# Kernel tuning notes

Hardware: AMD Instinct MI355X
Metric: run time of the kernel (lower is better)

Reference implementation:

```python
import jax, jax.numpy as jnp
import numpy as np

NUM_EXPERTS = 8
TOP_K = 2
D_IN = 1024
D_OUT = 1024
N_TOKENS = 8192


def setup_inputs() -> dict:
    key = jax.random.key(0)
    ks = jax.random.split(key, 7)
    s_in = 1.0 / np.sqrt(D_IN)
    s_out = 1.0 / np.sqrt(D_OUT)
    return {
        "x": jax.random.normal(ks[0], (N_TOKENS, D_IN), dtype=jnp.float32),
        # stacked expert params: fc1 [E, D_in, D_out], fc2 [E, D_out, D_out]
        "W1": jax.random.uniform(ks[1], (NUM_EXPERTS, D_IN, D_OUT), jnp.float32, -s_in, s_in),
        "b1": jax.random.uniform(ks[2], (NUM_EXPERTS, D_OUT), jnp.float32, -s_in, s_in),
        "W2": jax.random.uniform(ks[3], (NUM_EXPERTS, D_OUT, D_OUT), jnp.float32, -s_out, s_out),
        "b2": jax.random.uniform(ks[4], (NUM_EXPERTS, D_OUT), jnp.float32, -s_out, s_out),
        "Wg": jax.random.uniform(ks[5], (D_IN, NUM_EXPERTS), jnp.float32, -s_in, s_in),
        "bg": jax.random.uniform(ks[6], (NUM_EXPERTS,), jnp.float32, -s_in, s_in),
    }


def reference(x, W1, b1, W2, b2, Wg, bg):
    n = x.shape[0]
    # gating
    gate_logits = x @ Wg + bg                      # [N, E]
    gate_weights = jax.nn.softmax(gate_logits, axis=1)
    if TOP_K < NUM_EXPERTS:
        topk_vals, topk_idx = jax.lax.top_k(gate_weights, TOP_K)  # [N, K]
        rows = jnp.arange(n)[:, None]
        gate_weights = jnp.zeros_like(gate_weights).at[rows, topk_idx].set(topk_vals)
    # dense all-expert MLP fan-out (faithful to the original wasteful compute)
    h = jax.nn.relu(jnp.einsum('nd,edh->enh', x, W1) + b1[:, None, :])  # [E, N, H]
    y = jnp.einsum('enh,eho->eno', h, W2) + b2[:, None, :]               # [E, N, O]
    # weighted combine over experts
    out = jnp.einsum('ne,eno->no', gate_weights, y)                      # [N, O]
    return out
```

## Files before the change

kernel.cpp:

```cpp
#include <hip/hip_runtime.h>

#define NUM_E 8
#define N_TOK 8192
#define DIM 1024

typedef __attribute__((ext_vector_type(8))) short short8;
typedef __attribute__((ext_vector_type(4))) float f32x4;

__device__ __forceinline__ unsigned short f2bf(float f) {
  unsigned int u = __float_as_uint(f);
  u = (u + 0x7fffu + ((u >> 16) & 1u)) >> 16;
  return (unsigned short)u;
}

__device__ __forceinline__ void async16(const unsigned short* g, unsigned short* l) {
  __builtin_amdgcn_global_load_lds((const __attribute__((address_space(1))) void*)g,
                                   (__attribute__((address_space(3))) void*)l,
                                   16, 0, 0);
}

__global__ __launch_bounds__(256) void prep_kernel(
    const float* __restrict__ W1, const float* __restrict__ W2,
    unsigned short* __restrict__ W1T, unsigned short* __restrict__ W2T,
    const float* __restrict__ x, const float* __restrict__ Wg,
    const float* __restrict__ bg, int* __restrict__ tok_top,
    float2* __restrict__ tok_wts, unsigned short* __restrict__ xb) {
  __shared__ float s[64][65];
  if (blockIdx.x < 4096) {
    const int bx  = blockIdx.x;
    const int mat = bx >> 8;
    const int tk  = (bx >> 4) & 15;
    const int tn  = bx & 15;
    const float* src;
    unsigned short* dst;
    if (mat < 8) { src = W1 + (size_t)mat * (DIM * DIM); dst = W1T + (size_t)mat * (DIM * DIM); }
    else         { src = W2 + (size_t)(mat - 8) * (DIM * DIM); dst = W2T + (size_t)(mat - 8) * (DIM * DIM); }
    const int k0 = tk * 64, n0 = tn * 64;
    const int t = threadIdx.x;
    const int nr = t & 63, wr = t >> 6;
#pragma unroll
    for (int i = 0; i < 16; ++i) {
      int k = i * 4 + wr;
      s[nr][k] = src[(size_t)(k0 + k) * DIM + n0 + nr];
    }
    __syncthreads();
    const int kq = (t & 15) * 4, nw = t >> 4;
#pragma unroll
    for (int i = 0; i < 4; ++i) {
      int n = i * 16 + nw;
      ushort4 o;
      o.x = f2bf(s[n][kq + 0]); o.y = f2bf(s[n][kq + 1]);
      o.z = f2bf(s[n][kq + 2]); o.w = f2bf(s[n][kq + 3]);
      *(ushort4*)(dst + (size_t)(n0 + n) * DIM + k0 + kq) = o;
    }
  } else {
    const int wave = threadIdx.x >> 6;
    const int lane = threadIdx.x & 63;
    const int n = (blockIdx.x - 4096) * 4 + wave;
    const float4* xr = (const float4*)(x + (size_t)n * DIM);
    unsigned short* xbr = xb + (size_t)n * DIM;
    float acc[NUM_E];
#pragma unroll
    for (int e = 0; e < NUM_E; ++e) acc[e] = 0.f;
#pragma unroll
    for (int it = 0; it < 4; ++it) {
      float4 xv = xr[it * 64 + lane];
      const float4* wr = (const float4*)Wg + (size_t)(it * 256 + lane * 4) * 2;
      float xs[4] = {xv.x, xv.y, xv.z, xv.w};
      union { unsigned short u[4]; uint2 v; } oo;
      oo.u[0] = f2bf(xv.x); oo.u[1] = f2bf(xv.y);
      oo.u[2] = f2bf(xv.z); oo.u[3] = f2bf(xv.w);
      *(uint2*)(xbr + it * 256 + lane * 4) = oo.v;
#pragma unroll
      for (int dd = 0; dd < 4; ++dd) {
        float4 wa = wr[dd * 2 + 0];
        float4 wb = wr[dd * 2 + 1];
        acc[0] += xs[dd] * wa.x; acc[1] += xs[dd] * wa.y;
        acc[2] += xs[dd] * wa.z; acc[3] += xs[dd] * wa.w;
        acc[4] += xs[dd] * wb.x; acc[5] += xs[dd] * wb.y;
        acc[6] += xs[dd] * wb.z; acc[7] += xs[dd] * wb.w;
      }
    }
#pragma unroll
    for (int e = 0; e < NUM_E; ++e)
#pragma unroll
      for (int off = 32; off > 0; off >>= 1)
        acc[e] += __shfl_down(acc[e], off);
    if (lane == 0) {
      float p[NUM_E];
      float mx = -1e30f;
#pragma unroll
      for (int e = 0; e < NUM_E; ++e) { p[e] = acc[e] + bg[e]; mx = fmaxf(mx, p[e]); }
      float ss = 0.f;
#pragma unroll
      for (int e = 0; e < NUM_E; ++e) { p[e] = expf(p[e] - mx); ss += p[e]; }
      float inv = 1.f / ss;
      int i0 = 0;
#pragma unroll
      for (int e = 1; e < NUM_E; ++e) if (p[e] > p[i0]) i0 = e;
      int i1 = (i0 == 0) ? 1 : 0;
#pragma unroll
      for (int e = 0; e < NUM_E; ++e) if (e != i0 && p[e] > p[i1]) i1 = e;
      tok_top[n] = i0 | (i1 << 8);
      tok_wts[n] = make_float2(p[i0] * inv, p[i1] * inv);
    }
  }
}

__global__ __launch_bounds__(1024) void gate2_kernel(const int* __restrict__ tok_top,
                                                     const float2* __restrict__ tok_wts,
                                                     int* __restrict__ counts,
                                                     int* __restrict__ tok_idx,
                                                     float* __restrict__ tok_w) {
  const int e = blockIdx.x;
  const int t = threadIdx.x;
  const int lane = t & 63;
  const int wave = t >> 6;
  __shared__ int wsum[16];
  __shared__ int blocktot;
  int match[8];
  float w[8];
  int cnt = 0;
#pragma unroll
  for (int j = 0; j < 8; ++j) {
    int n = t * 8 + j;
    int top = tok_top[n];
    float2 ww = tok_wts[n];
    bool m0 = (top & 0xff) == e;
    bool m1 = ((top >> 8) & 0xff) == e;
    match[j] = (m0 || m1) ? 1 : 0;
    w[j] = m0 ? ww.x : ww.y;
    cnt += match[j];
  }
  int inc = cnt;
#pragma unroll
  for (int off = 1; off < 64; off <<= 1) {
    int v = __shfl_up(inc, off);
    if (lane >= off) inc += v;
  }
  if (lane == 63) wsum[wave] = inc;
  __syncthreads();
  if (t < 16) {
    int v = wsum[t];
    int s = v;
#pragma unroll
    for (int off = 1; off < 16; off <<= 1) {
      int u = __shfl_up(s, off);
      if (lane >= off) s += u;
    }
    wsum[t] = s - v;
    if (t == 15) blocktot = s;
  }
  __syncthreads();
  int slot = wsum[wave] + inc - cnt;
#pragma unroll
  for (int j = 0; j < 8; ++j) {
    if (match[j]) {
      tok_idx[e * N_TOK + slot] = t * 8 + j;
      tok_w[e * N_TOK + slot] = w[j];
      slot++;
    }
  }
  if (t == 0) counts[e] = blocktot;
}


template <bool FC1>
__global__ __launch_bounds__(256, 3) void moe_gemm_kernel(
    const unsigned short* __restrict__ A_src,
    const unsigned short* __restrict__ wT,
    const float* __restrict__ bias,
    const int* __restrict__ counts,
    const int* __restrict__ tok_idx,
    const float* __restrict__ tok_w,
    unsigned short* __restrict__ h_out,
    float* __restrict__ out)
{
  const int y = blockIdx.y;
  int e = -1, m0 = 0, base = 0;
  {
    int acc_tiles = 0, acc_rows = 0;
#pragma unroll
    for (int i = 0; i < NUM_E; ++i) {
      int c = counts[i];
      int t = (c + 127) >> 7;
      if (y >= acc_tiles && y < acc_tiles + t) {
        e = i; m0 = (y - acc_tiles) * 128; base = acc_rows;
      }
      acc_tiles += t;
      acc_rows += t * 128;
    }
  }
  if (e < 0) return;
  const int count = counts[e];
  const int n0 = blockIdx.x * 128;

  const int tid  = threadIdx.x;
  const int wave = tid >> 6;
  const int lane = tid & 63;
  const int l15  = lane & 15;
  const int quad = lane >> 4;
  const int wm   = wave & 1;
  const int wn   = wave >> 1;

  __shared__ unsigned short sA[2 * 4096];
  __shared__ unsigned short sB[2 * 4096];
  __shared__ int   s_tok[128];
  __shared__ float s_w[128];

  if (!FC1 && tid < 128) {
    int slot = m0 + tid;
    int cs = slot < count ? slot : count - 1;
    s_tok[tid] = tok_idx[e * N_TOK + cs];
    s_w[tid]   = slot < count ? tok_w[e * N_TOK + slot] : 0.f;
  }

  const int r0 = 32 * wave + l15;
  const int r1 = r0 + 16;
  size_t aOff0, aOff1;
  if (FC1) {
    int s0 = m0 + r0; s0 = s0 < count ? s0 : count - 1;
    int s1 = m0 + r1; s1 = s1 < count ? s1 : count - 1;
    aOff0 = (size_t)tok_idx[e * N_TOK + s0] * DIM;
    aOff1 = (size_t)tok_idx[e * N_TOK + s1] * DIM;
  } else {
    aOff0 = (size_t)(base + m0 + r0) * DIM;
    aOff1 = (size_t)(base + m0 + r1) * DIM;
  }
  const unsigned short* wte = wT + (size_t)e * DIM * DIM;
  const size_t bOff0 = (size_t)(n0 + r0) * DIM;
  const size_t bOff1 = (size_t)(n0 + r1) * DIM;
  const int kl = quad * 8;
  const int c0 = (2 * wave + 0) * 512;
  const int c1 = (2 * wave + 1) * 512;

  const f32x4 vzero = {0.f, 0.f, 0.f, 0.f};
  f32x4 acc[4][4];
#pragma unroll
  for (int i = 0; i < 4; ++i)
#pragma unroll
    for (int j = 0; j < 4; ++j) acc[i][j] = vzero;

  for (int k0 = 0; k0 < DIM; k0 += 64) {
    async16(A_src + aOff0 + k0 + kl,      &sA[c0]);
    async16(A_src + aOff1 + k0 + kl,      &sA[c1]);
    async16(A_src + aOff0 + k0 + 32 + kl, &sA[4096 + c0]);
    async16(A_src + aOff1 + k0 + 32 + kl, &sA[4096 + c1]);
    async16(wte + bOff0 + k0 + kl,        &sB[c0]);
    async16(wte + bOff1 + k0 + kl,        &sB[c1]);
    async16(wte + bOff0 + k0 + 32 + kl,   &sB[4096 + c0]);
    async16(wte + bOff1 + k0 + 32 + kl,   &sB[4096 + c1]);
    __syncthreads();
#pragma unroll
    for (int s = 0; s < 2; ++s) {
      short8 af[4], bfr[4];
#pragma unroll
      for (int i = 0; i < 4; ++i)
        af[i] = *(const short8*)&sA[s * 4096 + (wm * 4 + i) * 512 + lane * 8];
#pragma unroll
      for (int j = 0; j < 4; ++j)
        bfr[j] = *(const short8*)&sB[s * 4096 + (wn * 4 + j) * 512 + lane * 8];
#pragma unroll
      for (int i = 0; i < 4; ++i)
#pragma unroll
        for (int j = 0; j < 4; ++j)
          acc[i][j] = __builtin_amdgcn_mfma_f32_16x16x32_bf16(af[i], bfr[j], acc[i][j], 0, 0, 0);
    }
    __syncthreads();
  }

  float bv[4];
#pragma unroll
  for (int j = 0; j < 4; ++j)
    bv[j] = bias[e * DIM + n0 + (wn * 4 + j) * 16 + l15];

  if (FC1) {
#pragma unroll
    for (int i = 0; i < 4; ++i) {
      const int rbase = (wm * 4 + i) * 16 + quad * 4;
#pragma unroll
      for (int r = 0; r < 4; ++r) {
        const int slot = m0 + rbase + r;
        if (slot < count) {
          unsigned short* hp = h_out + (size_t)(base + slot) * DIM + n0;
#pragma unroll
          for (int j = 0; j < 4; ++j) {
            float v = acc[i][j][r] + bv[j];
            v = v > 0.f ? v : 0.f;
            hp[(wn * 4 + j) * 16 + l15] = f2bf(v);
          }
        }
      }
    }
  } else {
#pragma unroll
    for (int i = 0; i < 4; ++i) {
      const int rbase = (wm * 4 + i) * 16 + quad * 4;
#pragma unroll
      for (int r = 0; r < 4; ++r) {
        const int slot = m0 + rbase + r;
        if (slot < count) {
          const int rl = rbase + r;
          const int tok = s_tok[rl];
          const float w = s_w[rl];
          float* op = out + (size_t)tok * DIM + n0;
#pragma unroll
          for (int j = 0; j < 4; ++j) {
            float v = acc[i][j][r] + bv[j];
            atomicAdd(&op[(wn * 4 + j) * 16 + l15], w * v);
          }
        }
      }
    }
  }
}


extern "C" void kernel_launch(void* const* d_in, const int* in_sizes, int n_in,
                              void* d_out, int out_size, void* d_ws, size_t ws_size,
                              hipStream_t stream) {
  const float* x  = (const float*)d_in[0];
  const float* W1 = (const float*)d_in[1];
  const float* b1 = (const float*)d_in[2];
  const float* W2 = (const float*)d_in[3];
  const float* b2 = (const float*)d_in[4];
  const float* Wg = (const float*)d_in[5];
  const float* bg = (const float*)d_in[6];
  float* out = (float*)d_out;

  char* ws = (char*)d_ws;
  int*            counts  = (int*)(ws);
  int*            tok_idx = (int*)(ws + 1024);
  float*          tok_w   = (float*)(ws + 263168);
  unsigned short* xb      = (unsigned short*)(ws + 525312);
  unsigned short* w1t     = (unsigned short*)(ws + 525312 + 16777216ull);
  unsigned short* w2t     = (unsigned short*)(ws + 525312 + 2ull * 16777216ull);
  unsigned short* hb      = (unsigned short*)(ws + 525312 + 3ull * 16777216ull);
  size_t gate_off = 525312 + 3ull * 16777216ull + 35651584ull;
  int*            tok_top = (int*)(ws + gate_off);
  float2*         tok_wts = (float2*)(ws + gate_off + 32768);

  hipMemsetAsync(d_out, 0, (size_t)N_TOK * DIM * sizeof(float), stream);

  prep_kernel<<<4096 + 2048, 256, 0, stream>>>(W1, W2, w1t, w2t,
                                               x, Wg, bg, tok_top, tok_wts, xb);
  gate2_kernel<<<NUM_E, 1024, 0, stream>>>(tok_top, tok_wts, counts, tok_idx, tok_w);
  moe_gemm_kernel<true><<<dim3(8, 136), 256, 0, stream>>>(
      xb, w1t, b1, counts, tok_idx, tok_w, hb, nullptr);
  moe_gemm_kernel<false><<<dim3(8, 136), 256, 0, stream>>>(
      hb, w2t, b2, counts, tok_idx, tok_w, nullptr, out);
}
```

Measured before the change: 373.0 us.

## Double-buffer GEMM K-loop staging, vectorize weight transpose, raise occupancy hint

The GEMM main loop now ping-pongs two 32-wide K slices in shared memory, issuing async global-to-LDS loads for the next slice while MFMAs run on the current one, so load latency overlaps compute. The launch-bounds minimum-blocks hint goes from 3 to 4, which pressures the compiler toward fewer registers. The prep transpose now uses float4 global loads and 16-byte bf16 stores instead of scalar and 8-byte accesses. The risks are register spills from the tighter bound and LDS bank conflicts from the strided transpose writes.

```diff
diff --git a/kernel.cpp b/kernel.cpp
--- a/kernel.cpp
+++ b/kernel.cpp
@@ -37,21 +37,29 @@
     else         { src = W2 + (size_t)(mat - 8) * (DIM * DIM); dst = W2T + (size_t)(mat - 8) * (DIM * DIM); }
     const int k0 = tk * 64, n0 = tn * 64;
     const int t = threadIdx.x;
-    const int nr = t & 63, wr = t >> 6;
-#pragma unroll
-    for (int i = 0; i < 16; ++i) {
-      int k = i * 4 + wr;
-      s[nr][k] = src[(size_t)(k0 + k) * DIM + n0 + nr];
+    {
+      const int rr = t >> 4;
+      const int c4 = (t & 15) * 4;
+#pragma unroll
+      for (int i = 0; i < 4; ++i) {
+        const int k = i * 16 + rr;
+        float4 v = *(const float4*)&src[(size_t)(k0 + k) * DIM + n0 + c4];
+        s[c4 + 0][k] = v.x; s[c4 + 1][k] = v.y;
+        s[c4 + 2][k] = v.z; s[c4 + 3][k] = v.w;
+      }
     }
     __syncthreads();
-    const int kq = (t & 15) * 4, nw = t >> 4;
-#pragma unroll
-    for (int i = 0; i < 4; ++i) {
-      int n = i * 16 + nw;
-      ushort4 o;
-      o.x = f2bf(s[n][kq + 0]); o.y = f2bf(s[n][kq + 1]);
-      o.z = f2bf(s[n][kq + 2]); o.w = f2bf(s[n][kq + 3]);
-      *(ushort4*)(dst + (size_t)(n0 + n) * DIM + k0 + kq) = o;
+    {
+      const int kq = (t & 7) * 8;
+      const int nn = t >> 3;
+#pragma unroll
+      for (int r = 0; r < 2; ++r) {
+        const int n = r * 32 + nn;
+        union { unsigned short us[8]; uint4 v; } o;
+#pragma unroll
+        for (int j = 0; j < 8; ++j) o.us[j] = f2bf(s[n][kq + j]);
+        *(uint4*)(dst + (size_t)(n0 + n) * DIM + k0 + kq) = o.v;
+      }
     }
   } else {
     const int wave = threadIdx.x >> 6;
@@ -165,8 +173,34 @@
 }
 
 
+__device__ __forceinline__ void stage32(const unsigned short* A_src, size_t aOff0, size_t aOff1,
+                                        const unsigned short* wte, size_t bOff0, size_t bOff1,
+                                        int kk, int kl, int c0, int c1,
+                                        unsigned short* sa, unsigned short* sb) {
+  async16(A_src + aOff0 + kk + kl, sa + c0);
+  async16(A_src + aOff1 + kk + kl, sa + c1);
+  async16(wte + bOff0 + kk + kl, sb + c0);
+  async16(wte + bOff1 + kk + kl, sb + c1);
+}
+
+__device__ __forceinline__ void compute32(const unsigned short* sa, const unsigned short* sb,
+                                          int wm, int wn, int lane, f32x4 (&acc)[4][4]) {
+  short8 af[4], bfr[4];
+#pragma unroll
+  for (int i = 0; i < 4; ++i)
+    af[i] = *(const short8*)&sa[(wm * 4 + i) * 512 + lane * 8];
+#pragma unroll
+  for (int j = 0; j < 4; ++j)
+    bfr[j] = *(const short8*)&sb[(wn * 4 + j) * 512 + lane * 8];
+#pragma unroll
+  for (int i = 0; i < 4; ++i)
+#pragma unroll
+    for (int j = 0; j < 4; ++j)
+      acc[i][j] = __builtin_amdgcn_mfma_f32_16x16x32_bf16(af[i], bfr[j], acc[i][j], 0, 0, 0);
+}
+
 template <bool FC1>
-__global__ __launch_bounds__(256, 3) void moe_gemm_kernel(
+__global__ __launch_bounds__(256, 4) void moe_gemm_kernel(
     const unsigned short* __restrict__ A_src,
     const unsigned short* __restrict__ wT,
     const float* __restrict__ bias,
@@ -241,31 +275,17 @@
 #pragma unroll
     for (int j = 0; j < 4; ++j) acc[i][j] = vzero;
 
-  for (int k0 = 0; k0 < DIM; k0 += 64) {
-    async16(A_src + aOff0 + k0 + kl,      &sA[c0]);
-    async16(A_src + aOff1 + k0 + kl,      &sA[c1]);
-    async16(A_src + aOff0 + k0 + 32 + kl, &sA[4096 + c0]);
-    async16(A_src + aOff1 + k0 + 32 + kl, &sA[4096 + c1]);
-    async16(wte + bOff0 + k0 + kl,        &sB[c0]);
-    async16(wte + bOff1 + k0 + kl,        &sB[c1]);
-    async16(wte + bOff0 + k0 + 32 + kl,   &sB[4096 + c0]);
-    async16(wte + bOff1 + k0 + 32 + kl,   &sB[4096 + c1]);
+  stage32(A_src, aOff0, aOff1, wte, bOff0, bOff1, 0, kl, c0, c1, &sA[0], &sB[0]);
+  __syncthreads();
+  for (int kt = 0; kt < 32; kt += 2) {
+    stage32(A_src, aOff0, aOff1, wte, bOff0, bOff1, (kt + 1) * 32, kl, c0, c1,
+            &sA[4096], &sB[4096]);
+    compute32(&sA[0], &sB[0], wm, wn, lane, acc);
     __syncthreads();
-#pragma unroll
-    for (int s = 0; s < 2; ++s) {
-      short8 af[4], bfr[4];
-#pragma unroll
-      for (int i = 0; i < 4; ++i)
-        af[i] = *(const short8*)&sA[s * 4096 + (wm * 4 + i) * 512 + lane * 8];
-#pragma unroll
-      for (int j = 0; j < 4; ++j)
-        bfr[j] = *(const short8*)&sB[s * 4096 + (wn * 4 + j) * 512 + lane * 8];
-#pragma unroll
-      for (int i = 0; i < 4; ++i)
-#pragma unroll
-        for (int j = 0; j < 4; ++j)
-          acc[i][j] = __builtin_amdgcn_mfma_f32_16x16x32_bf16(af[i], bfr[j], acc[i][j], 0, 0, 0);
-    }
+    if (kt + 2 < 32)
+      stage32(A_src, aOff0, aOff1, wte, bOff0, bOff1, (kt + 2) * 32, kl, c0, c1,
+              &sA[0], &sB[0]);
+    compute32(&sA[4096], &sB[4096], wm, wn, lane, acc);
     __syncthreads();
   }
 
```

Result: slower. 382.6 us (+2.6%).
